# Performance work log

Measured on AMD Instinct MI355X. Metric: run time of the kernel, lower is better.

The kernel has to match this reference:

```python
import jax, jax.numpy as jnp
import numpy as np

D_MODEL = 4096
D_FF = 11008

def setup_inputs() -> dict:
    key = jax.random.key(0)
    k1, k2, k3, k4 = jax.random.split(key, 4)
    x = jax.random.normal(k1, (2, 2048, D_MODEL), dtype=jnp.float32)
    # Linear weights stored torch-style as [out_features, in_features]
    W_gate = jax.random.normal(k2, (D_FF, D_MODEL), dtype=jnp.float32) * (D_MODEL ** -0.5)
    W_up = jax.random.normal(k3, (D_FF, D_MODEL), dtype=jnp.float32) * (D_MODEL ** -0.5)
    W_down = jax.random.normal(k4, (D_MODEL, D_FF), dtype=jnp.float32) * (D_FF ** -0.5)
    return {"x": x, "W_gate": W_gate, "W_up": W_up, "W_down": W_down}

def reference(x, W_gate, W_up, W_down):
    out_shape = x.shape[:-1] + (W_down.shape[0],)
    xf = x.reshape(-1, x.shape[-1])                      # [T, d_model]
    up = jnp.einsum('td,fd->tf', xf, W_up)               # [T, d_ff]
    gate = jax.nn.silu(jnp.einsum('td,fd->tf', xf, W_gate))  # fused SiLU on gate proj
    h = gate * up                                        # [T, d_ff]
    y = jnp.einsum('tf,df->td', h, W_down)               # [T, d_model]
    return y.reshape(out_shape)
```

## Files before the change

### kernel.cpp

```cpp
#include <hip/hip_runtime.h>
#include <hip/hip_bf16.h>

#define D_MODEL 4096
#define D_FF    11008
#define NTOK    4096

typedef __attribute__((ext_vector_type(8))) short short8;
typedef __attribute__((ext_vector_type(4))) float f32x4;

__global__ void k_cvt(const float* __restrict__ in, __hip_bfloat16* __restrict__ out, int n8) {
    int i = blockIdx.x * blockDim.x + threadIdx.x;
    if (i >= n8) return;
    const float4* p = (const float4*)in;
    float4 v0 = p[(size_t)i * 2];
    float4 v1 = p[(size_t)i * 2 + 1];
    float vals[8] = {v0.x, v0.y, v0.z, v0.w, v1.x, v1.y, v1.z, v1.w};
    short8 o;
#pragma unroll
    for (int j = 0; j < 8; ++j) {
        __hip_bfloat16 b = __float2bfloat16(vals[j]);
        o[j] = *reinterpret_cast<short*>(&b);
    }
    *reinterpret_cast<short8*>(out + (size_t)i * 8) = o;
}

static __device__ __forceinline__ void stage_half(
    const __hip_bfloat16* g, int ld, __hip_bfloat16* lds, int tid)
{
#pragma unroll
    for (int s = 0; s < 2; ++s) {
        int ci = s * 512 + tid;
        int r  = ci >> 3;
        int c  = (ci & 7) ^ (r & 7);
        __builtin_amdgcn_global_load_lds(
            (const __attribute__((address_space(1))) void*)(g + (long)r * ld + c * 8),
            (__attribute__((address_space(3))) void*)(lds + ci * 8),
            16, 0, 0);
    }
}
static __device__ __forceinline__ int sw_off(int row, int kb) {
    return row * 64 + ((((kb >> 3) ^ (row & 7))) << 3);
}

#define MFMA16(a, b, c) __builtin_amdgcn_mfma_f32_16x16x32_bf16(a, b, c, 0, 0, 0)
#define VM4D do { if (pf) asm volatile("s_waitcnt vmcnt(4)" ::: "memory");     \
                  else    asm volatile("s_waitcnt vmcnt(0)" ::: "memory"); } while (0)

#define FPHASE(cA, cB, IQ, LOADB, STAGE, VMC)                                  \
    {                                                                          \
        short8 af[2][2];                                                       \
        _Pragma("unroll")                                                      \
        for (int ii = 0; ii < 2; ++ii)                                         \
            _Pragma("unroll")                                                  \
            for (int kk = 0; kk < 2; ++kk)                                     \
                af[ii][kk] = *reinterpret_cast<const short8*>(                 \
                    &(cA)[sw_off(wm * 128 + ((IQ) * 2 + ii) * 16 + r16,        \
                                 kk * 32 + g4 * 8)]);                          \
        if (LOADB) {                                                           \
            _Pragma("unroll")                                                  \
            for (int kk = 0; kk < 2; ++kk)                                     \
                _Pragma("unroll")                                              \
                for (int j = 0; j < 2; ++j) {                                  \
                    bg[kk][j] = *reinterpret_cast<const short8*>(              \
                        &(cB)[sw_off(wn * 32 + j * 16 + r16,                   \
                                     kk * 32 + g4 * 8)]);                      \
                    bu[kk][j] = *reinterpret_cast<const short8*>(              \
                        &(cB)[8192 + sw_off(wn * 32 + j * 16 + r16,            \
                                            kk * 32 + g4 * 8)]);               \
                }                                                              \
        }                                                                      \
        STAGE;                                                                 \
        VMC;                                                                   \
        if (LOADB) asm volatile("s_waitcnt lgkmcnt(8)" ::: "memory");          \
        __builtin_amdgcn_s_barrier();                                          \
        asm volatile("s_waitcnt lgkmcnt(0)" ::: "memory");                     \
        __builtin_amdgcn_sched_barrier(0);                                     \
        __builtin_amdgcn_s_setprio(1);                                         \
        _Pragma("unroll")                                                      \
        for (int ii = 0; ii < 2; ++ii)                                         \
            _Pragma("unroll")                                                  \
            for (int j = 0; j < 2; ++j) {                                      \
                accg[(IQ) * 2 + ii][j] = MFMA16(af[ii][0], bg[0][j],           \
                                                accg[(IQ) * 2 + ii][j]);       \
                accg[(IQ) * 2 + ii][j] = MFMA16(af[ii][1], bg[1][j],           \
                                                accg[(IQ) * 2 + ii][j]);       \
                accu[(IQ) * 2 + ii][j] = MFMA16(af[ii][0], bu[0][j],           \
                                                accu[(IQ) * 2 + ii][j]);       \
                accu[(IQ) * 2 + ii][j] = MFMA16(af[ii][1], bu[1][j],           \
                                                accu[(IQ) * 2 + ii][j]);       \
            }                                                                  \
        __builtin_amdgcn_s_setprio(0);                                         \
        __builtin_amdgcn_sched_barrier(0);                                     \
        __builtin_amdgcn_s_barrier();                                          \
    }

__global__ __launch_bounds__(512, 2)
void k_gateup(const __hip_bfloat16* __restrict__ X,
              const __hip_bfloat16* __restrict__ Wg,
              const __hip_bfloat16* __restrict__ Wu,
              __hip_bfloat16* __restrict__ H)
{
    extern __shared__ __hip_bfloat16 smem[];
    __hip_bfloat16* sA = smem;
    __hip_bfloat16* sB = smem + 32768;

    const int tid  = threadIdx.x;
    const int lane = tid & 63;
    const int wid  = tid >> 6;
    const int wm = wid >> 2, wn = wid & 3;
    const int r16 = lane & 15, g4 = lane >> 4;

    const int bid = blockIdx.x;
    const int o = (bid & 7) * 172 + (bid >> 3);
    const int n0 = (o >> 4) * 128;
    const int m0 = (o & 15) * 256;

    const int K = D_MODEL;
    const __hip_bfloat16* Ab = X  + (long)m0 * K;
    const __hip_bfloat16* Gb = Wg + (long)n0 * K;
    const __hip_bfloat16* Ub = Wu + (long)n0 * K;
    const long h1 = (long)128 * K;

    stage_half(Ab,        K, sA + 0,             tid);
    stage_half(Ab + h1,   K, sA + 8192,          tid);
    stage_half(Gb,        K, sB + 0,             tid);
    stage_half(Ub,        K, sB + 8192,          tid);
    stage_half(Gb + 64,   K, sB + 16384,         tid);
    stage_half(Ub + 64,   K, sB + 16384 + 8192,  tid);
    asm volatile("s_waitcnt vmcnt(4)" ::: "memory");
    __builtin_amdgcn_s_barrier();

    f32x4 accg[8][2], accu[8][2];
#pragma unroll
    for (int i = 0; i < 8; ++i)
#pragma unroll
        for (int j = 0; j < 2; ++j) {
            accg[i][j] = (f32x4){0.f, 0.f, 0.f, 0.f};
            accu[i][j] = (f32x4){0.f, 0.f, 0.f, 0.f};
        }

    const int nk = K >> 6;
    const int niter = nk >> 1;

    for (int it = 0; it < niter; ++it) {
        const bool pf = (it + 1 < niter);
        const long ko  = (long)(2 * it + 1) * 64;
        const long kn2 = (long)(2 * it + 2) * 64;
        const long kn3 = (long)(2 * it + 3) * 64;
        short8 bg[2][2], bu[2][2];
        {
            const __hip_bfloat16* cA = sA;
            const __hip_bfloat16* cB = sB;
            FPHASE(cA, cB, 0, 1,
                stage_half(Ab + ko,      K, sA + 16384,        tid), );
            FPHASE(cA, cB, 1, 0,
                stage_half(Ab + h1 + ko, K, sA + 16384 + 8192, tid), );
            FPHASE(cA, cB, 2, 0,
                if (pf) stage_half(Gb + kn2, K, sB + 0,    tid), );
            FPHASE(cA, cB, 3, 0,
                if (pf) stage_half(Ub + kn2, K, sB + 8192, tid), VM4D);
        }
        {
            const __hip_bfloat16* cA = sA + 16384;
            const __hip_bfloat16* cB = sB + 16384;
            FPHASE(cA, cB, 0, 1,
                if (pf) stage_half(Ab + kn2,      K, sA + 0,    tid), );
            FPHASE(cA, cB, 1, 0,
                if (pf) stage_half(Ab + h1 + kn2, K, sA + 8192, tid), );
            FPHASE(cA, cB, 2, 0,
                if (pf) stage_half(Gb + kn3, K, sB + 16384,        tid), );
            FPHASE(cA, cB, 3, 0,
                if (pf) stage_half(Ub + kn3, K, sB + 16384 + 8192, tid), VM4D);
        }
    }

#pragma unroll
    for (int i = 0; i < 8; ++i)
#pragma unroll
        for (int j = 0; j < 2; ++j)
#pragma unroll
            for (int r = 0; r < 4; ++r) {
                long row = m0 + wm * 128 + i * 16 + g4 * 4 + r;
                long col = n0 + wn * 32 + j * 16 + r16;
                float g = accg[i][j][r];
                float u = accu[i][j][r];
                float s = g / (1.f + __expf(-g));
                H[row * D_FF + col] = __float2bfloat16(s * u);
            }
}

#define DPHASE(cA, cB, IQ, LOADB, STAGE, VMC)                                  \
    {                                                                          \
        short8 af[2][2];                                                       \
        _Pragma("unroll")                                                      \
        for (int ii = 0; ii < 2; ++ii)                                         \
            _Pragma("unroll")                                                  \
            for (int kk = 0; kk < 2; ++kk)                                     \
                af[ii][kk] = *reinterpret_cast<const short8*>(                 \
                    &(cA)[sw_off(wm * 128 + ((IQ) * 2 + ii) * 16 + r16,        \
                                 kk * 32 + g4 * 8)]);                          \
        if (LOADB) {                                                           \
            _Pragma("unroll")                                                  \
            for (int kk = 0; kk < 2; ++kk)                                     \
                _Pragma("unroll")                                              \
                for (int j = 0; j < 4; ++j)                                    \
                    bfr[kk][j] = *reinterpret_cast<const short8*>(             \
                        &(cB)[sw_off(wn * 64 + j * 16 + r16,                   \
                                     kk * 32 + g4 * 8)]);                      \
        }                                                                      \
        STAGE;                                                                 \
        VMC;                                                                   \
        if (LOADB) asm volatile("s_waitcnt lgkmcnt(8)" ::: "memory");          \
        __builtin_amdgcn_s_barrier();                                          \
        asm volatile("s_waitcnt lgkmcnt(0)" ::: "memory");                     \
        __builtin_amdgcn_sched_barrier(0);                                     \
        __builtin_amdgcn_s_setprio(1);                                         \
        _Pragma("unroll")                                                      \
        for (int ii = 0; ii < 2; ++ii)                                         \
            _Pragma("unroll")                                                  \
            for (int j = 0; j < 4; ++j) {                                      \
                acc[(IQ) * 2 + ii][j] = MFMA16(af[ii][0], bfr[0][j],           \
                                               acc[(IQ) * 2 + ii][j]);         \
                acc[(IQ) * 2 + ii][j] = MFMA16(af[ii][1], bfr[1][j],           \
                                               acc[(IQ) * 2 + ii][j]);         \
            }                                                                  \
        __builtin_amdgcn_s_setprio(0);                                         \
        __builtin_amdgcn_sched_barrier(0);                                     \
        __builtin_amdgcn_s_barrier();                                          \
    }

__global__ __launch_bounds__(512, 2)
void k_down(const __hip_bfloat16* __restrict__ A,
            const __hip_bfloat16* __restrict__ B,
            float* __restrict__ Y)
{
    extern __shared__ __hip_bfloat16 smem[];
    __hip_bfloat16* sA = smem;
    __hip_bfloat16* sB = smem + 32768;

    const int tid  = threadIdx.x;
    const int lane = tid & 63;
    const int wid  = tid >> 6;
    const int wm = wid >> 2, wn = wid & 3;
    const int r16 = lane & 15, g4 = lane >> 4;

    const int bid = blockIdx.x;
    const int o = (bid & 7) * 32 + (bid >> 3);
    const int n0 = (o >> 4) << 8;
    const int m0 = (o & 15) << 8;

    const int K = D_FF;
    const int N = D_MODEL;
    const __hip_bfloat16* Ab = A + (long)m0 * K;
    const __hip_bfloat16* Bb = B + (long)n0 * K;
    const long h1 = (long)128 * K;

    stage_half(Ab,            K, sA + 0,             tid);
    stage_half(Ab + h1,       K, sA + 8192,          tid);
    stage_half(Bb,            K, sB + 0,             tid);
    stage_half(Bb + h1,       K, sB + 8192,          tid);
    stage_half(Bb + 64,       K, sB + 16384,         tid);
    stage_half(Bb + h1 + 64,  K, sB + 16384 + 8192,  tid);
    asm volatile("s_waitcnt vmcnt(4)" ::: "memory");
    __builtin_amdgcn_s_barrier();

    f32x4 acc[8][4];
#pragma unroll
    for (int i = 0; i < 8; ++i)
#pragma unroll
        for (int j = 0; j < 4; ++j)
            acc[i][j] = (f32x4){0.f, 0.f, 0.f, 0.f};

    const int nk = K >> 6;
    const int niter = nk >> 1;

    for (int it = 0; it < niter; ++it) {
        const bool pf = (it + 1 < niter);
        const long ko  = (long)(2 * it + 1) * 64;
        const long kn2 = (long)(2 * it + 2) * 64;
        const long kn3 = (long)(2 * it + 3) * 64;
        {
            const __hip_bfloat16* cA = sA;
            const __hip_bfloat16* cB = sB;
            short8 bfr[2][4];
            DPHASE(cA, cB, 0, 1,
                stage_half(Ab + ko,      K, sA + 16384,        tid), );
            DPHASE(cA, cB, 1, 0,
                stage_half(Ab + h1 + ko, K, sA + 16384 + 8192, tid), );
            DPHASE(cA, cB, 2, 0,
                if (pf) stage_half(Bb + kn2,      K, sB + 0,    tid), );
            DPHASE(cA, cB, 3, 0,
                if (pf) stage_half(Bb + h1 + kn2, K, sB + 8192, tid), VM4D);
        }
        {
            const __hip_bfloat16* cA = sA + 16384;
            const __hip_bfloat16* cB = sB + 16384;
            short8 bfr[2][4];
            DPHASE(cA, cB, 0, 1,
                if (pf) stage_half(Ab + kn2,      K, sA + 0,    tid), );
            DPHASE(cA, cB, 1, 0,
                if (pf) stage_half(Ab + h1 + kn2, K, sA + 8192, tid), );
            DPHASE(cA, cB, 2, 0,
                if (pf) stage_half(Bb + kn3,      K, sB + 16384, tid), );
            DPHASE(cA, cB, 3, 0,
                if (pf) stage_half(Bb + h1 + kn3, K, sB + 16384 + 8192, tid), VM4D);
        }
    }

#pragma unroll
    for (int i = 0; i < 8; ++i)
#pragma unroll
        for (int j = 0; j < 4; ++j)
#pragma unroll
            for (int r = 0; r < 4; ++r) {
                long row = m0 + wm * 128 + i * 16 + g4 * 4 + r;
                long col = n0 + wn * 64 + j * 16 + r16;
                Y[row * N + col] = acc[i][j][r];
            }
}

extern "C" void kernel_launch(void* const* d_in, const int* in_sizes, int n_in,
                              void* d_out, int out_size, void* d_ws, size_t ws_size,
                              hipStream_t stream) {
    const float* x  = (const float*)d_in[0];
    const float* wg = (const float*)d_in[1];
    const float* wu = (const float*)d_in[2];
    const float* wd = (const float*)d_in[3];
    float* y = (float*)d_out;

    char* ws = (char*)d_ws;
    const size_t szX = (size_t)NTOK * D_MODEL * 2;
    const size_t szW = (size_t)D_FF * D_MODEL * 2;
    __hip_bfloat16* Xb  = (__hip_bfloat16*)(ws);
    __hip_bfloat16* Wgb = (__hip_bfloat16*)(ws + szX);
    __hip_bfloat16* Wub = (__hip_bfloat16*)(ws + szX + szW);
    __hip_bfloat16* Wdb = (__hip_bfloat16*)(ws + szX + 2 * szW);
    __hip_bfloat16* Hb  = (__hip_bfloat16*)(ws + szX + 3 * szW);
    (void)ws_size; (void)out_size; (void)n_in; (void)in_sizes;

    const int SMEM = 131072;
    hipFuncSetAttribute((const void*)k_gateup, hipFuncAttributeMaxDynamicSharedMemorySize, SMEM);
    hipFuncSetAttribute((const void*)k_down,   hipFuncAttributeMaxDynamicSharedMemorySize, SMEM);

    const int nX = NTOK * D_MODEL / 8;
    const int nW = D_FF * D_MODEL / 8;
    k_cvt<<<(nX + 255) / 256, 256, 0, stream>>>(x, Xb, nX);
    k_cvt<<<(nW + 255) / 256, 256, 0, stream>>>(wg, Wgb, nW);
    k_cvt<<<(nW + 255) / 256, 256, 0, stream>>>(wu, Wub, nW);
    k_cvt<<<(nW + 255) / 256, 256, 0, stream>>>(wd, Wdb, nW);

    k_gateup<<<1376, 512, SMEM, stream>>>(Xb, Wgb, Wub, Hb);
    k_down<<<256, 512, SMEM, stream>>>(Hb, Wdb, y);
}
```

Before: 1.049 ms.

## Fuse fp32-to-bf16 weight conversion into GEMM tile loads

Drops the three standalone conversion kernels for W_gate, W_up and W_down. The gate/up and down GEMMs now read fp32 weight tiles straight into registers, convert them to bf16, and write them to swizzled LDS, with the load/convert/store steps spread across the pipeline phases. This removes a full read-and-write pass over all weights plus three launches. In exchange, the GEMMs fetch twice as many weight bytes per tile, the weight loads go through VGPRs instead of direct global-to-LDS copies, and the extra 64 registers may cause spills or lower occupancy.

Result: slower. 2.765 ms (+163.5%).

```diff
diff --git a/kernel.cpp b/kernel.cpp
--- a/kernel.cpp
+++ b/kernel.cpp
@@ -42,11 +42,43 @@
     return row * 64 + ((((kb >> 3) ^ (row & 7))) << 3);
 }
 
+#define LOADW(wreg, P0, P1, KOFF)                                              \
+    _Pragma("unroll")                                                          \
+    for (int q = 0; q < 2; ++q) {                                              \
+        const float* srcw = ((q == 0) ? (P0) : (P1)) + (KOFF);                 \
+        _Pragma("unroll")                                                      \
+        for (int s = 0; s < 2; ++s) {                                          \
+            int ci = s * 512 + tid;                                            \
+            int rr = ci >> 3, cc = (ci & 7) ^ (rr & 7);                        \
+            const f32x4* gp = reinterpret_cast<const f32x4*>(                  \
+                srcw + (long)rr * K + cc * 8);                                 \
+            wreg[q * 4 + s * 2 + 0] = gp[0];                                   \
+            wreg[q * 4 + s * 2 + 1] = gp[1];                                   \
+        }                                                                      \
+    }
+
+#define WRITEW(wreg, ldsbase)                                                  \
+    _Pragma("unroll")                                                          \
+    for (int q = 0; q < 2; ++q)                                                \
+        _Pragma("unroll")                                                      \
+        for (int s = 0; s < 2; ++s) {                                          \
+            int ci = s * 512 + tid;                                            \
+            short8 pk;                                                         \
+            _Pragma("unroll")                                                  \
+            for (int e = 0; e < 4; ++e) {                                      \
+                __hip_bfloat16 b0 = __float2bfloat16(wreg[q*4+s*2+0][e]);      \
+                __hip_bfloat16 b1 = __float2bfloat16(wreg[q*4+s*2+1][e]);      \
+                pk[e]     = *reinterpret_cast<short*>(&b0);                    \
+                pk[4 + e] = *reinterpret_cast<short*>(&b1);                    \
+            }                                                                  \
+            *reinterpret_cast<short8*>((ldsbase) + (q ? 8192 : 0) + ci * 8) = pk; \
+        }
+
 #define MFMA16(a, b, c) __builtin_amdgcn_mfma_f32_16x16x32_bf16(a, b, c, 0, 0, 0)
-#define VM4D do { if (pf) asm volatile("s_waitcnt vmcnt(4)" ::: "memory");     \
-                  else    asm volatile("s_waitcnt vmcnt(0)" ::: "memory"); } while (0)
-
-#define FPHASE(cA, cB, IQ, LOADB, STAGE, VMC)                                  \
+#define VMW(pfflag) do { if (pfflag) asm volatile("s_waitcnt vmcnt(8)" ::: "memory"); \
+                         else        asm volatile("s_waitcnt vmcnt(0)" ::: "memory"); } while (0)
+
+#define FPHASE(cA, cB, IQ, LOADB, STAGE)                                       \
     {                                                                          \
         short8 af[2][2];                                                       \
         _Pragma("unroll")                                                      \
@@ -70,7 +102,6 @@
                 }                                                              \
         }                                                                      \
         STAGE;                                                                 \
-        VMC;                                                                   \
         if (LOADB) asm volatile("s_waitcnt lgkmcnt(8)" ::: "memory");          \
         __builtin_amdgcn_s_barrier();                                          \
         asm volatile("s_waitcnt lgkmcnt(0)" ::: "memory");                     \
@@ -96,8 +127,8 @@
 
 __global__ __launch_bounds__(512, 2)
 void k_gateup(const __hip_bfloat16* __restrict__ X,
-              const __hip_bfloat16* __restrict__ Wg,
-              const __hip_bfloat16* __restrict__ Wu,
+              const float* __restrict__ Wg,
+              const float* __restrict__ Wu,
               __hip_bfloat16* __restrict__ H)
 {
     extern __shared__ __hip_bfloat16 smem[];
@@ -116,18 +147,20 @@
     const int m0 = (o & 15) * 256;
 
     const int K = D_MODEL;
-    const __hip_bfloat16* Ab = X  + (long)m0 * K;
-    const __hip_bfloat16* Gb = Wg + (long)n0 * K;
-    const __hip_bfloat16* Ub = Wu + (long)n0 * K;
+    const __hip_bfloat16* Ab = X + (long)m0 * K;
+    const float* G32 = Wg + (long)n0 * K;
+    const float* U32 = Wu + (long)n0 * K;
     const long h1 = (long)128 * K;
 
-    stage_half(Ab,        K, sA + 0,             tid);
-    stage_half(Ab + h1,   K, sA + 8192,          tid);
-    stage_half(Gb,        K, sB + 0,             tid);
-    stage_half(Ub,        K, sB + 8192,          tid);
-    stage_half(Gb + 64,   K, sB + 16384,         tid);
-    stage_half(Ub + 64,   K, sB + 16384 + 8192,  tid);
-    asm volatile("s_waitcnt vmcnt(4)" ::: "memory");
+    f32x4 wA[8], wB[8];
+
+    stage_half(Ab,      K, sA + 0,    tid);
+    stage_half(Ab + h1, K, sA + 8192, tid);
+    LOADW(wA, G32, U32, 0)
+    asm volatile("s_waitcnt vmcnt(0)" ::: "memory");
+    WRITEW(wA, sB)
+    LOADW(wB, G32, U32, 64)
+    asm volatile("s_waitcnt lgkmcnt(0)" ::: "memory");
     __builtin_amdgcn_s_barrier();
 
     f32x4 accg[8][2], accu[8][2];
@@ -144,33 +177,26 @@
 
     for (int it = 0; it < niter; ++it) {
         const bool pf = (it + 1 < niter);
-        const long ko  = (long)(2 * it + 1) * 64;
-        const long kn2 = (long)(2 * it + 2) * 64;
-        const long kn3 = (long)(2 * it + 3) * 64;
+        const long kA1 = (long)(2 * it + 1) * 64;
+        const long kA2 = (long)(2 * it + 2) * 64;
+        const long kW2 = (long)(2 * it + 2) * 64;
+        const long kW3 = (long)(2 * it + 3) * 64;
         short8 bg[2][2], bu[2][2];
         {
             const __hip_bfloat16* cA = sA;
             const __hip_bfloat16* cB = sB;
-            FPHASE(cA, cB, 0, 1,
-                stage_half(Ab + ko,      K, sA + 16384,        tid), );
-            FPHASE(cA, cB, 1, 0,
-                stage_half(Ab + h1 + ko, K, sA + 16384 + 8192, tid), );
-            FPHASE(cA, cB, 2, 0,
-                if (pf) stage_half(Gb + kn2, K, sB + 0,    tid), );
-            FPHASE(cA, cB, 3, 0,
-                if (pf) stage_half(Ub + kn2, K, sB + 8192, tid), VM4D);
+            FPHASE(cA, cB, 0, 1, stage_half(Ab + kA1,      K, sA + 16384,        tid));
+            FPHASE(cA, cB, 1, 0, stage_half(Ab + h1 + kA1, K, sA + 16384 + 8192, tid));
+            FPHASE(cA, cB, 2, 0, if (pf) LOADW(wA, G32, U32, kW2));
+            FPHASE(cA, cB, 3, 0, { VMW(pf); WRITEW(wB, sB + 16384) });
         }
         {
             const __hip_bfloat16* cA = sA + 16384;
             const __hip_bfloat16* cB = sB + 16384;
-            FPHASE(cA, cB, 0, 1,
-                if (pf) stage_half(Ab + kn2,      K, sA + 0,    tid), );
-            FPHASE(cA, cB, 1, 0,
-                if (pf) stage_half(Ab + h1 + kn2, K, sA + 8192, tid), );
-            FPHASE(cA, cB, 2, 0,
-                if (pf) stage_half(Gb + kn3, K, sB + 16384,        tid), );
-            FPHASE(cA, cB, 3, 0,
-                if (pf) stage_half(Ub + kn3, K, sB + 16384 + 8192, tid), VM4D);
+            FPHASE(cA, cB, 0, 1, if (pf) stage_half(Ab + kA2,      K, sA + 0,    tid));
+            FPHASE(cA, cB, 1, 0, if (pf) stage_half(Ab + h1 + kA2, K, sA + 8192, tid));
+            FPHASE(cA, cB, 2, 0, if (pf) LOADW(wB, G32, U32, kW3));
+            FPHASE(cA, cB, 3, 0, { if (pf) { VMW(true); WRITEW(wA, sB) } });
         }
     }
 
@@ -189,7 +215,7 @@
             }
 }
 
-#define DPHASE(cA, cB, IQ, LOADB, STAGE, VMC)                                  \
+#define DPHASE(cA, cB, IQ, LOADB, STAGE)                                       \
     {                                                                          \
         short8 af[2][2];                                                       \
         _Pragma("unroll")                                                      \
@@ -209,7 +235,6 @@
                                      kk * 32 + g4 * 8)]);                      \
         }                                                                      \
         STAGE;                                                                 \
-        VMC;                                                                   \
         if (LOADB) asm volatile("s_waitcnt lgkmcnt(8)" ::: "memory");          \
         __builtin_amdgcn_s_barrier();                                          \
         asm volatile("s_waitcnt lgkmcnt(0)" ::: "memory");                     \
@@ -231,7 +256,7 @@
 
 __global__ __launch_bounds__(512, 2)
 void k_down(const __hip_bfloat16* __restrict__ A,
-            const __hip_bfloat16* __restrict__ B,
+            const float* __restrict__ Wd,
             float* __restrict__ Y)
 {
     extern __shared__ __hip_bfloat16 smem[];
@@ -252,16 +277,19 @@
     const int K = D_FF;
     const int N = D_MODEL;
     const __hip_bfloat16* Ab = A + (long)m0 * K;
-    const __hip_bfloat16* Bb = B + (long)n0 * K;
+    const float* B032 = Wd + (long)n0 * K;
+    const float* B132 = Wd + (long)(n0 + 128) * K;
     const long h1 = (long)128 * K;
 
-    stage_half(Ab,            K, sA + 0,             tid);
-    stage_half(Ab + h1,       K, sA + 8192,          tid);
-    stage_half(Bb,            K, sB + 0,             tid);
-    stage_half(Bb + h1,       K, sB + 8192,          tid);
-    stage_half(Bb + 64,       K, sB + 16384,         tid);
-    stage_half(Bb + h1 + 64,  K, sB + 16384 + 8192,  tid);
-    asm volatile("s_waitcnt vmcnt(4)" ::: "memory");
+    f32x4 wA[8], wB[8];
+
+    stage_half(Ab,      K, sA + 0,    tid);
+    stage_half(Ab + h1, K, sA + 8192, tid);
+    LOADW(wA, B032, B132, 0)
+    asm volatile("s_waitcnt vmcnt(0)" ::: "memory");
+    WRITEW(wA, sB)
+    LOADW(wB, B032, B132, 64)
+    asm volatile("s_waitcnt lgkmcnt(0)" ::: "memory");
     __builtin_amdgcn_s_barrier();
 
     f32x4 acc[8][4];
@@ -276,34 +304,26 @@
 
     for (int it = 0; it < niter; ++it) {
         const bool pf = (it + 1 < niter);
-        const long ko  = (long)(2 * it + 1) * 64;
-        const long kn2 = (long)(2 * it + 2) * 64;
-        const long kn3 = (long)(2 * it + 3) * 64;
+        const long kA1 = (long)(2 * it + 1) * 64;
+        const long kA2 = (long)(2 * it + 2) * 64;
+        const long kW2 = (long)(2 * it + 2) * 64;
+        const long kW3 = (long)(2 * it + 3) * 64;
+        short8 bfr[2][4];
         {
             const __hip_bfloat16* cA = sA;
             const __hip_bfloat16* cB = sB;
-            short8 bfr[2][4];
-            DPHASE(cA, cB, 0, 1,
-                stage_half(Ab + ko,      K, sA + 16384,        tid), );
-            DPHASE(cA, cB, 1, 0,
-                stage_half(Ab + h1 + ko, K, sA + 16384 + 8192, tid), );
-            DPHASE(cA, cB, 2, 0,
-                if (pf) stage_half(Bb + kn2,      K, sB + 0,    tid), );
-            DPHASE(cA, cB, 3, 0,
-                if (pf) stage_half(Bb + h1 + kn2, K, sB + 8192, tid), VM4D);
+            DPHASE(cA, cB, 0, 1, stage_half(Ab + kA1,      K, sA + 16384,        tid));
+            DPHASE(cA, cB, 1, 0, stage_half(Ab + h1 + kA1, K, sA + 16384 + 8192, tid));
+            DPHASE(cA, cB, 2, 0, if (pf) LOADW(wA, B032, B132, kW2));
+            DPHASE(cA, cB, 3, 0, { VMW(pf); WRITEW(wB, sB + 16384) });
         }
         {
             const __hip_bfloat16* cA = sA + 16384;
             const __hip_bfloat16* cB = sB + 16384;
-            short8 bfr[2][4];
-            DPHASE(cA, cB, 0, 1,
-                if (pf) stage_half(Ab + kn2,      K, sA + 0,    tid), );
-            DPHASE(cA, cB, 1, 0,
-                if (pf) stage_half(Ab + h1 + kn2, K, sA + 8192, tid), );
-            DPHASE(cA, cB, 2, 0,
-                if (pf) stage_half(Bb + kn3,      K, sB + 16384, tid), );
-            DPHASE(cA, cB, 3, 0,
-                if (pf) stage_half(Bb + h1 + kn3, K, sB + 16384 + 8192, tid), VM4D);
+            DPHASE(cA, cB, 0, 1, if (pf) stage_half(Ab + kA2,      K, sA + 0,    tid));
+            DPHASE(cA, cB, 1, 0, if (pf) stage_half(Ab + h1 + kA2, K, sA + 8192, tid));
+            DPHASE(cA, cB, 2, 0, if (pf) LOADW(wB, B032, B132, kW3));
+            DPHASE(cA, cB, 3, 0, { if (pf) { VMW(true); WRITEW(wA, sB) } });
         }
     }
 
@@ -330,12 +350,8 @@
 
     char* ws = (char*)d_ws;
     const size_t szX = (size_t)NTOK * D_MODEL * 2;
-    const size_t szW = (size_t)D_FF * D_MODEL * 2;
-    __hip_bfloat16* Xb  = (__hip_bfloat16*)(ws);
-    __hip_bfloat16* Wgb = (__hip_bfloat16*)(ws + szX);
-    __hip_bfloat16* Wub = (__hip_bfloat16*)(ws + szX + szW);
-    __hip_bfloat16* Wdb = (__hip_bfloat16*)(ws + szX + 2 * szW);
-    __hip_bfloat16* Hb  = (__hip_bfloat16*)(ws + szX + 3 * szW);
+    __hip_bfloat16* Xb = (__hip_bfloat16*)(ws);
+    __hip_bfloat16* Hb = (__hip_bfloat16*)(ws + szX);
     (void)ws_size; (void)out_size; (void)n_in; (void)in_sizes;
 
     const int SMEM = 131072;
@@ -343,12 +359,8 @@
     hipFuncSetAttribute((const void*)k_down,   hipFuncAttributeMaxDynamicSharedMemorySize, SMEM);
 
     const int nX = NTOK * D_MODEL / 8;
-    const int nW = D_FF * D_MODEL / 8;
     k_cvt<<<(nX + 255) / 256, 256, 0, stream>>>(x, Xb, nX);
-    k_cvt<<<(nW + 255) / 256, 256, 0, stream>>>(wg, Wgb, nW);
-    k_cvt<<<(nW + 255) / 256, 256, 0, stream>>>(wu, Wub, nW);
-    k_cvt<<<(nW + 255) / 256, 256, 0, stream>>>(wd, Wdb, nW);
-
-    k_gateup<<<1376, 512, SMEM, stream>>>(Xb, Wgb, Wub, Hb);
-    k_down<<<256, 512, SMEM, stream>>>(Hb, Wdb, y);
-}
+
+    k_gateup<<<1376, 512, SMEM, stream>>>(Xb, wg, wu, Hb);
+    k_down<<<256, 512, SMEM, stream>>>(Hb, wd, y);
+}
```

## Fuse W_down bf16 conversion into gate/up kernel tail blocks and remap tiles per XCD

Applied to the files above, without the earlier changes.

Removes the separate conversion launch for W_down and instead appends 160 extra blocks to the gate/up GEMM grid that convert W_down to bf16 with a grid-stride loop. The goal is to overlap that memory-bound conversion with the compute-bound GEMM and fill the last partial wave. The block-to-tile mapping also changes so that each XCD owns two fixed M row-blocks and walks N, which is meant to improve L2 reuse of X within each XCD. Risks: the conversion blocks compete with GEMM blocks for bandwidth and CU slots, and the new mapping changes how weights are reused across XCDs.

Result: faster. 1.004 ms (-4.4%).

```diff
diff --git a/kernel.cpp b/kernel.cpp
--- a/kernel.cpp
+++ b/kernel.cpp
@@ -98,22 +98,44 @@
 void k_gateup(const __hip_bfloat16* __restrict__ X,
               const __hip_bfloat16* __restrict__ Wg,
               const __hip_bfloat16* __restrict__ Wu,
-              __hip_bfloat16* __restrict__ H)
+              __hip_bfloat16* __restrict__ H,
+              const float* __restrict__ Wd32,
+              __hip_bfloat16* __restrict__ Wdb)
 {
     extern __shared__ __hip_bfloat16 smem[];
     __hip_bfloat16* sA = smem;
     __hip_bfloat16* sB = smem + 32768;
 
-    const int tid  = threadIdx.x;
+    const int tid = threadIdx.x;
+    const int bid = blockIdx.x;
+
+    if (bid >= 1376) {
+        const long total8 = (long)D_MODEL * D_FF / 8;
+        const long stride = 160L * 512;
+        for (long i = (long)(bid - 1376) * 512 + tid; i < total8; i += stride) {
+            const float4* p = (const float4*)(Wd32 + i * 8);
+            float4 v0 = p[0], v1 = p[1];
+            float vals[8] = {v0.x, v0.y, v0.z, v0.w, v1.x, v1.y, v1.z, v1.w};
+            short8 oo;
+#pragma unroll
+            for (int j = 0; j < 8; ++j) {
+                __hip_bfloat16 b = __float2bfloat16(vals[j]);
+                oo[j] = *reinterpret_cast<short*>(&b);
+            }
+            *reinterpret_cast<short8*>(Wdb + i * 8) = oo;
+        }
+        return;
+    }
+
     const int lane = tid & 63;
     const int wid  = tid >> 6;
     const int wm = wid >> 2, wn = wid & 3;
     const int r16 = lane & 15, g4 = lane >> 4;
 
-    const int bid = blockIdx.x;
-    const int o = (bid & 7) * 172 + (bid >> 3);
-    const int n0 = (o >> 4) * 128;
-    const int m0 = (o & 15) * 256;
+    const int xcd = bid & 7;
+    const int o   = bid >> 3;
+    const int n0 = (o >> 1) * 128;
+    const int m0 = (xcd * 2 + (o & 1)) * 256;
 
     const int K = D_MODEL;
     const __hip_bfloat16* Ab = X  + (long)m0 * K;
@@ -139,7 +161,7 @@
             accu[i][j] = (f32x4){0.f, 0.f, 0.f, 0.f};
         }
 
-    const int nk = K >> 6;
+    const int nk = D_MODEL >> 6;
     const int niter = nk >> 1;
 
     for (int it = 0; it < niter; ++it) {
@@ -347,8 +369,7 @@
     k_cvt<<<(nX + 255) / 256, 256, 0, stream>>>(x, Xb, nX);
     k_cvt<<<(nW + 255) / 256, 256, 0, stream>>>(wg, Wgb, nW);
     k_cvt<<<(nW + 255) / 256, 256, 0, stream>>>(wu, Wub, nW);
-    k_cvt<<<(nW + 255) / 256, 256, 0, stream>>>(wd, Wdb, nW);
-
-    k_gateup<<<1376, 512, SMEM, stream>>>(Xb, Wgb, Wub, Hb);
+
+    k_gateup<<<1536, 512, SMEM, stream>>>(Xb, Wgb, Wub, Hb, wd, Wdb);
     k_down<<<256, 512, SMEM, stream>>>(Hb, Wdb, y);
 }
```
